# Kernel tuning notes

Hardware: AMD Instinct MI355X
Metric: run time of the kernel (lower is better)

## Reference

```python
import jax, jax.numpy as jnp
import numpy as np
from jax.scipy.special import logsumexp

B, T, V, E, H, L = 64, 256, 50000, 256, 256, 9


def setup_inputs() -> dict:
    key = jax.random.key(0)
    ks = jax.random.split(key, 10)
    lengths = jax.random.randint(ks[0], (B,), T // 2, T + 1)
    pm = jnp.arange(T)[None, :] < lengths[:, None]  # valid-token mask, padding at tail
    inp = jnp.where(pm, jax.random.randint(ks[1], (B, T), 1, V), 0).astype(jnp.int32)
    tags = jnp.where(pm, jax.random.randint(ks[2], (B, T), 0, L), 0).astype(jnp.int32)
    s = 0.05
    emb = jax.random.normal(ks[3], (V, E)) * s
    Wf = jax.random.normal(ks[4], (E, 4 * H)) * s
    Uf = jax.random.normal(ks[5], (H, 4 * H)) * s
    bf = jnp.zeros((4 * H,))
    Wb = jax.random.normal(ks[6], (E, 4 * H)) * s
    Ub = jax.random.normal(ks[7], (H, 4 * H)) * s
    bb = jnp.zeros((4 * H,))
    Wd = jax.random.normal(ks[8], (2 * H, L)) * s
    bd = jnp.zeros((L,))
    trans = jax.random.uniform(ks[9], (L, L))
    return dict(inp=inp, tags=tags, emb=emb, Wf=Wf, Uf=Uf, bf=bf,
                Wb=Wb, Ub=Ub, bb=bb, Wd=Wd, bd=bd, trans=trans)


def _lstm(x, mask, W, U, b):
    """Keras-style LSTM with masking (state + output carried through masked steps).
    x: [B,T,E], mask: [B,T] bool -> [B,T,H]."""
    h0 = jnp.zeros((x.shape[0], H), x.dtype)
    c0 = h0

    def step(carry, xm):
        h, c = carry
        xt, mt = xm
        z = xt @ W + h @ U + b  # [B,4H], gate order i,f,g,o (Keras)
        i, f, g, o = jnp.split(z, 4, axis=-1)
        c_new = jax.nn.sigmoid(f) * c + jax.nn.sigmoid(i) * jnp.tanh(g)
        h_new = jax.nn.sigmoid(o) * jnp.tanh(c_new)
        m = mt[:, None]
        h = jnp.where(m, h_new, h)
        c = jnp.where(m, c_new, c)
        return (h, c), h

    _, hs = jax.lax.scan(step, (h0, c0), (x.transpose(1, 0, 2), mask.T))
    return hs.transpose(1, 0, 2)


def _crf_log_likelihood(pot, tags, seq_lens, trans):
    """tfa.text.crf_log_likelihood: sequence_score - log_norm. pot: [B,T,L]."""
    Bv, Tv, Lv = pot.shape
    tmask = (jnp.arange(Tv)[None, :] < seq_lens[:, None]).astype(pot.dtype)
    unary = jnp.sum(jnp.take_along_axis(pot, tags[..., None], axis=-1)[..., 0] * tmask, axis=1)
    pmask = (jnp.arange(Tv - 1)[None, :] < (seq_lens - 1)[:, None]).astype(pot.dtype)
    binary = jnp.sum(trans[tags[:, :-1], tags[:, 1:]] * pmask, axis=1)

    # forward algorithm; alpha frozen once t >= seq_len (tfa uses dynamic_rnn semantics)
    def step(carry, pot_t):
        alpha, t = carry
        new = pot_t + logsumexp(alpha[:, :, None] + trans[None], axis=1)  # [B,L]
        alpha = jnp.where((t < seq_lens)[:, None], new, alpha)
        return (alpha, t + 1), None

    (alpha, _), _ = jax.lax.scan(step, (pot[:, 0, :], jnp.int32(1)),
                                 pot[:, 1:].transpose(1, 0, 2))
    log_norm = logsumexp(alpha, axis=-1)
    return unary + binary - log_norm


def reference(inp, tags, emb, Wf, Uf, bf, Wb, Ub, bb, Wd, bd, trans):
    mask = inp != 0
    seq_lens = jnp.sum(mask.astype(jnp.int32), axis=-1)
    x = jnp.take(emb, inp, axis=0)  # [B,T,E]; dropout is identity (inference)
    hf = _lstm(x, mask, Wf, Uf, bf)
    hb = _lstm(x[:, ::-1], mask[:, ::-1], Wb, Ub, bb)[:, ::-1]
    pot = jnp.concatenate([hf, hb], axis=-1) @ Wd + bd  # [B,T,L]
    ll = _crf_log_likelihood(pot, tags, seq_lens, trans)
    loss = -jnp.mean(ll / seq_lens.astype(pot.dtype))
    return pot, seq_lens, loss
```

## Files before the change

### kernel.cpp

```cpp
#include <hip/hip_runtime.h>

#define B_ 64
#define T_ 256
#define E_ 256
#define H_ 256
#define G4 1024
#define L_ 9

typedef __attribute__((ext_vector_type(8))) short bf16x8;
typedef __attribute__((ext_vector_type(4))) float f32x4;
typedef __attribute__((ext_vector_type(4))) unsigned uint4v;
typedef _Float16 half2v __attribute__((ext_vector_type(2)));

__device__ __forceinline__ ushort f2bf(float x){
  unsigned u = __float_as_uint(x);
  unsigned r = (u + 0x7FFFu + ((u >> 16) & 1u)) >> 16;
  return (ushort)r;
}
__device__ __forceinline__ float bf2f(unsigned u16v){
  return __uint_as_float(u16v << 16);
}
__device__ __forceinline__ float fsig(float x){
  return __builtin_amdgcn_rcpf(1.f + __expf(-x));
}
__device__ __forceinline__ float ftanh(float x){
  return 1.f - 2.f * __builtin_amdgcn_rcpf(__expf(2.f * x) + 1.f);
}
__device__ __forceinline__ int sdot4(unsigned a, unsigned b, int c){
#if __has_builtin(__builtin_amdgcn_sdot4)
  return __builtin_amdgcn_sdot4((int)a, (int)b, c, false);
#else
  int r = c;
  #pragma unroll
  for (int j = 0; j < 4; j++){
    int av = (int)(signed char)((a >> (8 * j)) & 0xFF);
    int bv = (int)(signed char)((b >> (8 * j)) & 0xFF);
    r += av * bv;
  }
  return r;
#endif
}

__global__ void k_prep(const int* __restrict__ inp, const float* __restrict__ emb,
                       const float* __restrict__ Wf, const float* __restrict__ Wb,
                       const float* __restrict__ Uf, const float* __restrict__ Ub,
                       ushort* __restrict__ WT, unsigned* __restrict__ Uq,
                       float* __restrict__ su, ushort* __restrict__ X,
                       int* __restrict__ lens, float* __restrict__ out_len){
  int bid = blockIdx.x, tid = threadIdx.x;
  if (bid < 2048){
    int idx = bid * 256 + tid;
    int dir = idx >> 18; int rem = idx & 262143;
    int np = rem >> 8, k = rem & 255;
    int c = ((np & 3) << 8) | (np >> 2);
    const float* W = dir ? Wb : Wf;
    WT[idx] = f2bf(W[k * G4 + c]);
  } else if (bid < 2080){
    int idx = bid - 2048;
    int dir = idx >> 4, blk = idx & 15;
    int c0 = blk * 64;
    int g = blk >> 2, u0 = (blk & 3) * 64;
    const float* U = dir ? Ub : Uf;
    int cp = tid & 63, ph = tid >> 6;
    __shared__ float redA[4][64];
    __shared__ float rs[64];
    __shared__ unsigned qbuf[64][64];
    float am = 0.f;
    for (int kk = 0; kk < 64; ++kk){
      float v = U[(size_t)(kk * 4 + ph) * G4 + c0 + cp];
      am = fmaxf(am, fabsf(v));
    }
    redA[ph][cp] = am;
    __syncthreads();
    if (tid < 64){
      float m = fmaxf(fmaxf(redA[0][tid], redA[1][tid]),
                      fmaxf(redA[2][tid], redA[3][tid]));
      float mm = fmaxf(m, 1e-20f);
      rs[tid] = 127.f / mm;
      su[dir * 1024 + c0 + tid] = mm * (1.f / 127.f);
    }
    __syncthreads();
    float rsv = rs[cp];
    for (int w = 0; w < 16; ++w){
      int kq = ph * 16 + w;
      unsigned word = 0;
      #pragma unroll
      for (int j = 0; j < 4; ++j){
        float v = U[(size_t)(kq * 4 + j) * G4 + c0 + cp];
        int q = __float2int_rn(v * rsv);
        q = max(-127, min(127, q));
        word |= ((unsigned)(q & 0xFF)) << (8 * j);
      }
      qbuf[kq][cp] = word;
    }
    __syncthreads();
    {
      int uu = tid >> 2, part = tid & 3;
      int kh = part >> 1, hs = part & 1;
      unsigned* dst = Uq + dir * 65536 + (u0 + uu) * 256 + kh * 128 + g * 32 + hs * 16;
      #pragma unroll
      for (int w4 = 0; w4 < 4; ++w4){
        int kb = kh * 32 + hs * 16 + w4 * 4;
        uint4 val;
        val.x = qbuf[kb + 0][uu];
        val.y = qbuf[kb + 1][uu];
        val.z = qbuf[kb + 2][uu];
        val.w = qbuf[kb + 3][uu];
        *(uint4*)(dst + w4 * 4) = val;
      }
    }
  } else if (bid < 4128){
    int idx = (bid - 2080) * 256 + tid;
    int m = idx >> 5, koff = (idx & 31) * 8;
    int tok = inp[m];
    const float* src = emb + (size_t)tok * E_ + koff;
    float4 a = *(const float4*)src;
    float4 b = *(const float4*)(src + 4);
    uint4 o;
    o.x = (unsigned)f2bf(a.x) | ((unsigned)f2bf(a.y) << 16);
    o.y = (unsigned)f2bf(a.z) | ((unsigned)f2bf(a.w) << 16);
    o.z = (unsigned)f2bf(b.x) | ((unsigned)f2bf(b.y) << 16);
    o.w = (unsigned)f2bf(b.z) | ((unsigned)f2bf(b.w) << 16);
    *(uint4*)(X + m * E_ + koff) = o;
  } else {
    int w = tid >> 6, lane = tid & 63;
    int b = (bid - 4128) * 4 + w;
    int c = 0;
    for (int t = lane; t < T_; t += 64) c += (inp[b * T_ + t] != 0);
    for (int off = 32; off; off >>= 1) c += __shfl_xor(c, off);
    if (lane == 0){ lens[b] = c; out_len[b] = (float)c; }
  }
}

__global__ __launch_bounds__(256) void k_gemm(const ushort* __restrict__ X,
        const ushort* __restrict__ WT, const float* __restrict__ bf_,
        const float* __restrict__ bb_, ushort* __restrict__ Zpf, ushort* __restrict__ Zpb){
  int zi = blockIdx.z;
  const ushort* wt = WT + zi * 262144;
  const float* bias = zi ? bb_ : bf_;
  ushort* Zp = zi ? Zpb : Zpf;
  int m0 = blockIdx.x * 128, n0 = blockIdx.y * 128;
  __shared__ ushort As[128 * 32];
  __shared__ ushort Bs[128 * 32];
  int tid = threadIdx.x;
  int lane = tid & 63, w = tid >> 6;
  int wr = w >> 1, wc = w & 1;
  int srow = lane >> 2, skq = lane & 3;
  int lr = lane & 15, kf8 = (lane >> 4) * 8;
  f32x4 acc[4][4] = {};
  for (int k0 = 0; k0 < E_; k0 += 32){
    #pragma unroll
    for (int j = 0; j < 2; j++){
      int rg = (w * 2 + j) * 16;
      const ushort* ga = X  + (size_t)(m0 + rg + srow) * E_ + k0 + skq * 8;
      const ushort* gb = wt + (size_t)(n0 + rg + srow) * E_ + k0 + skq * 8;
      __builtin_amdgcn_global_load_lds(
          (const __attribute__((address_space(1))) unsigned*)ga,
          (__attribute__((address_space(3))) unsigned*)&As[rg * 32], 16, 0, 0);
      __builtin_amdgcn_global_load_lds(
          (const __attribute__((address_space(1))) unsigned*)gb,
          (__attribute__((address_space(3))) unsigned*)&Bs[rg * 32], 16, 0, 0);
    }
    __syncthreads();
    bf16x8 af[4], bfr[4];
    #pragma unroll
    for (int i = 0; i < 4; i++){
      af[i]  = *(const bf16x8*)&As[(wr * 64 + i * 16 + lr) * 32 + kf8];
      bfr[i] = *(const bf16x8*)&Bs[(wc * 64 + i * 16 + lr) * 32 + kf8];
    }
    #pragma unroll
    for (int i = 0; i < 4; i++)
      #pragma unroll
      for (int j = 0; j < 4; j++)
        acc[i][j] = __builtin_amdgcn_mfma_f32_16x16x32_bf16(af[i], bfr[j], acc[i][j], 0, 0, 0);
    __syncthreads();
  }
  int crow = (lane >> 4) * 4;
  #pragma unroll
  for (int j = 0; j < 4; j++){
    int col = n0 + wc * 64 + j * 16 + lr;
    float bv = bias[((col & 3) << 8) | (col >> 2)];
    #pragma unroll
    for (int i = 0; i < 4; i++){
      int rbase = m0 + wr * 64 + i * 16 + crow;
      #pragma unroll
      for (int r = 0; r < 4; r++)
        Zp[(size_t)(rbase + r) * 1024 + col] = f2bf(acc[i][j][r] + bv);
    }
  }
}

__global__ __launch_bounds__(512, 2) void k_recur13(
    const ushort* __restrict__ Zpf, const ushort* __restrict__ Zpb,
    const unsigned* __restrict__ Uq, const float* __restrict__ su,
    const int* __restrict__ lens, ushort* __restrict__ hf16, ushort* __restrict__ hb16){
  int bid = blockIdx.x;
  int dir = bid >> 6, b = bid & 63;
  const uint2* Zp = (const uint2*)(dir ? Zpb : Zpf);
  ushort* H = dir ? hb16 : hf16;
  int tid = threadIdx.x;
  int u = tid >> 1, khalf = tid & 1;
  float sc0 = su[dir * 1024 +        u] * (1.f / 127.f);
  float sc1 = su[dir * 1024 + 256 +  u] * (1.f / 127.f);
  float sc2 = su[dir * 1024 + 512 +  u] * (1.f / 127.f);
  float sc3 = su[dir * 1024 + 768 +  u] * (1.f / 127.f);
  int alen = lens[b];

  uint4v uq[4][8];
  {
    const unsigned* p = Uq + dir * 65536 + u * 256 + khalf * 128;
    #pragma unroll
    for (int g = 0; g < 4; g++)
      #pragma unroll
      for (int i = 0; i < 8; i++)
        asm volatile("global_load_dwordx4 %0, %1, off"
                     : "=v"(uq[g][i]) : "v"(p + g * 32 + i * 4));
    asm volatile("s_waitcnt vmcnt(0)" ::: "memory");
    __builtin_amdgcn_sched_barrier(0);
  }

  __shared__ unsigned hq[2][64];
  if (tid < 128) ((unsigned*)hq)[tid] = 0u;
  __syncthreads();

  float c_st = 0.f, h_st = 0.f;
  int t0 = dir ? 255 : 0;
  uint2 zw = Zp[(size_t)(b * 256 + t0) * 256 + u];

  for (int s_ = 0; s_ < 256; ++s_){
    int t = dir ? (255 - s_) : s_;
    int tn = dir ? (t - 1) : (t + 1);
    int cur = s_ & 1, nxt = cur ^ 1;
    uint2 zw_n = uint2{0u, 0u};
    if (s_ < 255) zw_n = Zp[(size_t)(b * 256 + tn) * 256 + u];
    const uint4* hp = (const uint4*)&hq[cur][khalf * 32];
    uint4 hv[8];
    #pragma unroll
    for (int i = 0; i < 8; i++) hv[i] = hp[i];
    __builtin_amdgcn_sched_barrier(0);
    int a0 = 0, a1 = 0, a2 = 0, a3 = 0;
    #pragma unroll
    for (int i = 0; i < 8; i++){
      uint4 hvv = hv[i];
      a0 = sdot4(uq[0][i][0], hvv.x, a0);  a0 = sdot4(uq[0][i][1], hvv.y, a0);
      a0 = sdot4(uq[0][i][2], hvv.z, a0);  a0 = sdot4(uq[0][i][3], hvv.w, a0);
      a1 = sdot4(uq[1][i][0], hvv.x, a1);  a1 = sdot4(uq[1][i][1], hvv.y, a1);
      a1 = sdot4(uq[1][i][2], hvv.z, a1);  a1 = sdot4(uq[1][i][3], hvv.w, a1);
      a2 = sdot4(uq[2][i][0], hvv.x, a2);  a2 = sdot4(uq[2][i][1], hvv.y, a2);
      a2 = sdot4(uq[2][i][2], hvv.z, a2);  a2 = sdot4(uq[2][i][3], hvv.w, a2);
      a3 = sdot4(uq[3][i][0], hvv.x, a3);  a3 = sdot4(uq[3][i][1], hvv.y, a3);
      a3 = sdot4(uq[3][i][2], hvv.z, a3);  a3 = sdot4(uq[3][i][3], hvv.w, a3);
    }
    a0 += __shfl_xor(a0, 1);
    a1 += __shfl_xor(a1, 1);
    a2 += __shfl_xor(a2, 1);
    a3 += __shfl_xor(a3, 1);
    float zi = bf2f(zw.x & 0xffffu) + (float)a0 * sc0;
    float zf = bf2f(zw.x >> 16)     + (float)a1 * sc1;
    float zg = bf2f(zw.y & 0xffffu) + (float)a2 * sc2;
    float zo = bf2f(zw.y >> 16)     + (float)a3 * sc3;
    if (t < alen){
      c_st = fsig(zf) * c_st + fsig(zi) * ftanh(zg);
      h_st = fsig(zo) * ftanh(c_st);
    }
    if (khalf == 0){
      int ri = __float2int_rn(h_st * 127.f);
      ((char*)hq[nxt])[u] = (char)ri;
      H[(size_t)(b * 256 + t) * H_ + u] = f2bf(h_st);
    }
    __syncthreads();
    zw = zw_n;
  }
}

__global__ __launch_bounds__(256) void k_pot(const ushort* __restrict__ hf16,
        const ushort* __restrict__ hb16, const float* __restrict__ Wd,
        const float* __restrict__ bd, float* __restrict__ out, int* __restrict__ cnt){
  if (blockIdx.x == 0 && threadIdx.x == 0) *cnt = 0;
  int lane = threadIdx.x & 63, wid = threadIdx.x >> 6;
  int m = blockIdx.x * 4 + wid;
  uint2 ua = *(const uint2*)&hf16[(size_t)m * H_ + lane * 4];
  uint2 ub = *(const uint2*)&hb16[(size_t)m * H_ + lane * 4];
  float av[4] = {bf2f(ua.x & 0xFFFFu), bf2f(ua.x >> 16), bf2f(ua.y & 0xFFFFu), bf2f(ua.y >> 16)};
  float bv[4] = {bf2f(ub.x & 0xFFFFu), bf2f(ub.x >> 16), bf2f(ub.y & 0xFFFFu), bf2f(ub.y >> 16)};
  float acc[9];
  #pragma unroll
  for (int l = 0; l < 9; l++) acc[l] = 0.f;
  #pragma unroll
  for (int i = 0; i < 4; i++){
    int r = lane * 4 + i;
    #pragma unroll
    for (int l = 0; l < 9; l++)
      acc[l] += av[i] * Wd[r * 9 + l] + bv[i] * Wd[(H_ + r) * 9 + l];
  }
  #pragma unroll
  for (int off = 32; off; off >>= 1)
    #pragma unroll
    for (int l = 0; l < 9; l++) acc[l] += __shfl_xor(acc[l], off);
  if (lane == 0){
    #pragma unroll
    for (int l = 0; l < 9; l++) out[(size_t)m * 9 + l] = acc[l] + bd[l];
  }
}

__global__ void k_post(const float* __restrict__ out, const int* __restrict__ tags,
                       const float* __restrict__ trans, const int* __restrict__ lens,
                       float* __restrict__ lln, int* cnt, float* __restrict__ loss_out){
  int b = blockIdx.x, lane = threadIdx.x;
  int len = lens[b];
  const float* pot = out + (size_t)b * T_ * 9;
  float up = 0.f, bp = 0.f;
  for (int t = lane; t < T_; t += 64){
    int tg = tags[b * T_ + t];
    if (t < len) up += pot[t * 9 + tg];
    if (t + 1 < len){
      int tg2 = tags[b * T_ + t + 1];
      bp += trans[tg * 9 + tg2];
    }
  }
  for (int off = 32; off; off >>= 1){ up += __shfl_xor(up, off); bp += __shfl_xor(bp, off); }
  float alpha = 0.f;
  if (lane < 9){
    float tr[9];
    #pragma unroll
    for (int i = 0; i < 9; i++) tr[i] = trans[i * 9 + lane];
    alpha = pot[lane];
    for (int t = 1; t < T_; ++t){
      float v[9];
      #pragma unroll
      for (int i = 0; i < 9; i++) v[i] = __shfl(alpha, i) + tr[i];
      float mx = v[0];
      #pragma unroll
      for (int i = 1; i < 9; i++) mx = fmaxf(mx, v[i]);
      float sum = 0.f;
      #pragma unroll
      for (int i = 0; i < 9; i++) sum += __expf(v[i] - mx);
      float an = pot[t * 9 + lane] + mx + __logf(sum);
      if (t < len) alpha = an;
    }
  }
  float mx2 = -3.4e38f;
  for (int i = 0; i < 9; i++){ float a = __shfl(alpha, i); mx2 = fmaxf(mx2, a); }
  float s2 = 0.f;
  for (int i = 0; i < 9; i++){ float a = __shfl(alpha, i); s2 += __expf(a - mx2); }
  float lse = mx2 + __logf(s2);
  __shared__ int lastf;
  if (lane == 0){
    __hip_atomic_store(&lln[b], (up + bp - lse) / (float)len,
                       __ATOMIC_RELAXED, __HIP_MEMORY_SCOPE_AGENT);
    int old = __hip_atomic_fetch_add(cnt, 1, __ATOMIC_ACQ_REL, __HIP_MEMORY_SCOPE_AGENT);
    lastf = (old == 63);
  }
  __syncthreads();
  if (lastf){
    float v = __hip_atomic_load(&lln[lane], __ATOMIC_RELAXED, __HIP_MEMORY_SCOPE_AGENT);
    for (int off = 32; off; off >>= 1) v += __shfl_xor(v, off);
    if (lane == 0) loss_out[0] = -v * (1.f / 64.f);
  }
}

extern "C" void kernel_launch(void* const* d_in, const int* in_sizes, int n_in,
                              void* d_out, int out_size, void* d_ws, size_t ws_size,
                              hipStream_t stream) {
  (void)in_sizes; (void)n_in; (void)out_size; (void)ws_size;
  const int*   inp   = (const int*)  d_in[0];
  const int*   tags  = (const int*)  d_in[1];
  const float* emb   = (const float*)d_in[2];
  const float* Wf    = (const float*)d_in[3];
  const float* Uf    = (const float*)d_in[4];
  const float* bfv   = (const float*)d_in[5];
  const float* Wb    = (const float*)d_in[6];
  const float* Ub    = (const float*)d_in[7];
  const float* bbv   = (const float*)d_in[8];
  const float* Wd    = (const float*)d_in[9];
  const float* bd    = (const float*)d_in[10];
  const float* trans = (const float*)d_in[11];
  float* out = (float*)d_out;

  char* ws = (char*)d_ws;
  unsigned* Uq   = (unsigned*)(ws);
  float*    su   = (float*)   (ws + 524288);
  ushort*   WT16 = (ushort*)  (ws + 1048576);
  ushort*   Xbf  = (ushort*)  (ws + 2097152);
  int*      cnt  = (int*)     (ws + 2097152);
  ushort*   Zpf  = (ushort*)  (ws + 10485760);
  ushort*   Zpb  = (ushort*)  (ws + 44040192);
  ushort*   hf16 = (ushort*)  (ws + 77594624);
  ushort*   hb16 = (ushort*)  (ws + 85983232);
  int*      lens = (int*)     (ws + 94371840);
  float*    lln  = (float*)   (ws + 94372096);

  k_prep<<<4144, 256, 0, stream>>>(inp, emb, Wf, Wb, Uf, Ub, WT16, Uq, su, Xbf,
                                   lens, out + 147456);
  k_gemm<<<dim3(128, 8, 2), 256, 0, stream>>>(Xbf, WT16, bfv, bbv, Zpf, Zpb);
  k_recur13<<<128, 512, 0, stream>>>(Zpf, Zpb, Uq, su, lens, hf16, hb16);
  k_pot<<<4096, 256, 0, stream>>>(hf16, hb16, Wd, bd, out, cnt);
  k_post<<<64, 64, 0, stream>>>(out, tags, trans, lens, lln, cnt, out + 147520);
}
```

Baseline: 392.7 us.

## Fuse potential projection with CRF tail and stage GEMM output through LDS

Merges the emission-potential projection and the CRF forward/loss kernel into a single per-sequence kernel. Each block keeps its potentials in shared memory, so one launch and the global round-trip of potentials go away. The GEMM epilogue now writes the bf16 tile to padded LDS and then stores coalesced 16-byte rows instead of scattered 2-byte stores. The fused kernel runs only 64 blocks, so the projection gets far less parallelism than the 4096-block version had, and the GEMM block uses about 34KB more LDS. The counter reset moves into the prep kernel.

```diff
diff --git a/kernel.cpp b/kernel.cpp
--- a/kernel.cpp
+++ b/kernel.cpp
@@ -46,7 +46,8 @@
                        const float* __restrict__ Uf, const float* __restrict__ Ub,
                        ushort* __restrict__ WT, unsigned* __restrict__ Uq,
                        float* __restrict__ su, ushort* __restrict__ X,
-                       int* __restrict__ lens, float* __restrict__ out_len){
+                       int* __restrict__ lens, float* __restrict__ out_len,
+                       int* __restrict__ cnt){
   int bid = blockIdx.x, tid = threadIdx.x;
   if (bid < 2048){
     int idx = bid * 256 + tid;
@@ -123,6 +124,7 @@
     o.w = (unsigned)f2bf(b.z) | ((unsigned)f2bf(b.w) << 16);
     *(uint4*)(X + m * E_ + koff) = o;
   } else {
+    if (bid == 4128 && tid == 0) cnt[0] = 0;
     int w = tid >> 6, lane = tid & 63;
     int b = (bid - 4128) * 4 + w;
     int c = 0;
@@ -142,6 +144,7 @@
   int m0 = blockIdx.x * 128, n0 = blockIdx.y * 128;
   __shared__ ushort As[128 * 32];
   __shared__ ushort Bs[128 * 32];
+  __shared__ ushort Cs[128 * 136];
   int tid = threadIdx.x;
   int lane = tid & 63, w = tid >> 6;
   int wr = w >> 1, wc = w & 1;
@@ -178,15 +181,23 @@
   int crow = (lane >> 4) * 4;
   #pragma unroll
   for (int j = 0; j < 4; j++){
-    int col = n0 + wc * 64 + j * 16 + lr;
-    float bv = bias[((col & 3) << 8) | (col >> 2)];
+    int col = wc * 64 + j * 16 + lr;
+    float bv = bias[(((n0 + col) & 3) << 8) | ((n0 + col) >> 2)];
     #pragma unroll
     for (int i = 0; i < 4; i++){
-      int rbase = m0 + wr * 64 + i * 16 + crow;
+      int rbase = wr * 64 + i * 16 + crow;
       #pragma unroll
       for (int r = 0; r < 4; r++)
-        Zp[(size_t)(rbase + r) * 1024 + col] = f2bf(acc[i][j][r] + bv);
-    }
+        Cs[(rbase + r) * 136 + col] = f2bf(acc[i][j][r] + bv);
+    }
+  }
+  __syncthreads();
+  #pragma unroll
+  for (int P = 0; P < 8; P++){
+    int row = P * 16 + (tid >> 4);
+    int seg = tid & 15;
+    uint4 v = *(const uint4*)&Cs[row * 136 + seg * 8];
+    *(uint4*)&Zp[(size_t)(m0 + row) * 1024 + n0 + seg * 8] = v;
   }
 }
 
@@ -273,89 +284,96 @@
   }
 }
 
-__global__ __launch_bounds__(256) void k_pot(const ushort* __restrict__ hf16,
-        const ushort* __restrict__ hb16, const float* __restrict__ Wd,
-        const float* __restrict__ bd, float* __restrict__ out, int* __restrict__ cnt){
-  if (blockIdx.x == 0 && threadIdx.x == 0) *cnt = 0;
-  int lane = threadIdx.x & 63, wid = threadIdx.x >> 6;
-  int m = blockIdx.x * 4 + wid;
-  uint2 ua = *(const uint2*)&hf16[(size_t)m * H_ + lane * 4];
-  uint2 ub = *(const uint2*)&hb16[(size_t)m * H_ + lane * 4];
-  float av[4] = {bf2f(ua.x & 0xFFFFu), bf2f(ua.x >> 16), bf2f(ua.y & 0xFFFFu), bf2f(ua.y >> 16)};
-  float bv[4] = {bf2f(ub.x & 0xFFFFu), bf2f(ub.x >> 16), bf2f(ub.y & 0xFFFFu), bf2f(ub.y >> 16)};
-  float acc[9];
-  #pragma unroll
-  for (int l = 0; l < 9; l++) acc[l] = 0.f;
-  #pragma unroll
-  for (int i = 0; i < 4; i++){
-    int r = lane * 4 + i;
-    #pragma unroll
-    for (int l = 0; l < 9; l++)
-      acc[l] += av[i] * Wd[r * 9 + l] + bv[i] * Wd[(H_ + r) * 9 + l];
-  }
-  #pragma unroll
-  for (int off = 32; off; off >>= 1)
-    #pragma unroll
-    for (int l = 0; l < 9; l++) acc[l] += __shfl_xor(acc[l], off);
-  if (lane == 0){
-    #pragma unroll
-    for (int l = 0; l < 9; l++) out[(size_t)m * 9 + l] = acc[l] + bd[l];
-  }
-}
-
-__global__ void k_post(const float* __restrict__ out, const int* __restrict__ tags,
-                       const float* __restrict__ trans, const int* __restrict__ lens,
-                       float* __restrict__ lln, int* cnt, float* __restrict__ loss_out){
-  int b = blockIdx.x, lane = threadIdx.x;
-  int len = lens[b];
-  const float* pot = out + (size_t)b * T_ * 9;
-  float up = 0.f, bp = 0.f;
-  for (int t = lane; t < T_; t += 64){
-    int tg = tags[b * T_ + t];
-    if (t < len) up += pot[t * 9 + tg];
-    if (t + 1 < len){
-      int tg2 = tags[b * T_ + t + 1];
-      bp += trans[tg * 9 + tg2];
-    }
-  }
-  for (int off = 32; off; off >>= 1){ up += __shfl_xor(up, off); bp += __shfl_xor(bp, off); }
-  float alpha = 0.f;
-  if (lane < 9){
-    float tr[9];
-    #pragma unroll
-    for (int i = 0; i < 9; i++) tr[i] = trans[i * 9 + lane];
-    alpha = pot[lane];
-    for (int t = 1; t < T_; ++t){
-      float v[9];
-      #pragma unroll
-      for (int i = 0; i < 9; i++) v[i] = __shfl(alpha, i) + tr[i];
-      float mx = v[0];
-      #pragma unroll
-      for (int i = 1; i < 9; i++) mx = fmaxf(mx, v[i]);
-      float sum = 0.f;
-      #pragma unroll
-      for (int i = 0; i < 9; i++) sum += __expf(v[i] - mx);
-      float an = pot[t * 9 + lane] + mx + __logf(sum);
-      if (t < len) alpha = an;
-    }
-  }
-  float mx2 = -3.4e38f;
-  for (int i = 0; i < 9; i++){ float a = __shfl(alpha, i); mx2 = fmaxf(mx2, a); }
-  float s2 = 0.f;
-  for (int i = 0; i < 9; i++){ float a = __shfl(alpha, i); s2 += __expf(a - mx2); }
-  float lse = mx2 + __logf(s2);
-  __shared__ int lastf;
-  if (lane == 0){
-    __hip_atomic_store(&lln[b], (up + bp - lse) / (float)len,
-                       __ATOMIC_RELAXED, __HIP_MEMORY_SCOPE_AGENT);
-    int old = __hip_atomic_fetch_add(cnt, 1, __ATOMIC_ACQ_REL, __HIP_MEMORY_SCOPE_AGENT);
-    lastf = (old == 63);
+__global__ __launch_bounds__(1024) void k_tail(
+    const ushort* __restrict__ hf16, const ushort* __restrict__ hb16,
+    const float* __restrict__ Wd, const float* __restrict__ bd,
+    const int* __restrict__ tags, const float* __restrict__ trans,
+    const int* __restrict__ lens, float* __restrict__ out,
+    float* __restrict__ lln, int* cnt, float* __restrict__ loss_out){
+  int b = blockIdx.x;
+  int tid = threadIdx.x;
+  int lane = tid & 63, w = tid >> 6;
+  __shared__ float potS[256][9];
+  for (int it = 0; it < 16; ++it){
+    int r = w * 16 + it;
+    size_t m = (size_t)b * 256 + r;
+    uint2 ua = *(const uint2*)&hf16[m * 256 + lane * 4];
+    uint2 ub = *(const uint2*)&hb16[m * 256 + lane * 4];
+    float av[4] = {bf2f(ua.x & 0xFFFFu), bf2f(ua.x >> 16), bf2f(ua.y & 0xFFFFu), bf2f(ua.y >> 16)};
+    float bv[4] = {bf2f(ub.x & 0xFFFFu), bf2f(ub.x >> 16), bf2f(ub.y & 0xFFFFu), bf2f(ub.y >> 16)};
+    float acc[9];
+    #pragma unroll
+    for (int l = 0; l < 9; l++) acc[l] = 0.f;
+    #pragma unroll
+    for (int i = 0; i < 4; i++){
+      int rr = lane * 4 + i;
+      #pragma unroll
+      for (int l = 0; l < 9; l++)
+        acc[l] += av[i] * Wd[rr * 9 + l] + bv[i] * Wd[(H_ + rr) * 9 + l];
+    }
+    #pragma unroll
+    for (int off = 32; off; off >>= 1)
+      #pragma unroll
+      for (int l = 0; l < 9; l++) acc[l] += __shfl_xor(acc[l], off);
+    if (lane == 0){
+      #pragma unroll
+      for (int l = 0; l < 9; l++){
+        float v = acc[l] + bd[l];
+        potS[r][l] = v;
+        out[m * 9 + l] = v;
+      }
+    }
   }
   __syncthreads();
-  if (lastf){
-    float v = __hip_atomic_load(&lln[lane], __ATOMIC_RELAXED, __HIP_MEMORY_SCOPE_AGENT);
-    for (int off = 32; off; off >>= 1) v += __shfl_xor(v, off);
-    if (lane == 0) loss_out[0] = -v * (1.f / 64.f);
+  if (tid < 64){
+    int len = lens[b];
+    float up = 0.f, bp = 0.f;
+    for (int t = lane; t < T_; t += 64){
+      int tg = tags[b * T_ + t];
+      if (t < len) up += potS[t][tg];
+      if (t + 1 < len){
+        int tg2 = tags[b * T_ + t + 1];
+        bp += trans[tg * 9 + tg2];
+      }
+    }
+    for (int off = 32; off; off >>= 1){ up += __shfl_xor(up, off); bp += __shfl_xor(bp, off); }
+    float alpha = 0.f;
+    if (lane < 9){
+      float tr[9];
+      #pragma unroll
+      for (int i = 0; i < 9; i++) tr[i] = trans[i * 9 + lane];
+      alpha = potS[0][lane];
+      for (int t = 1; t < T_; ++t){
+        float v[9];
+        #pragma unroll
+        for (int i = 0; i < 9; i++) v[i] = __shfl(alpha, i) + tr[i];
+        float mx = v[0];
+        #pragma unroll
+        for (int i = 1; i < 9; i++) mx = fmaxf(mx, v[i]);
+        float sum = 0.f;
+        #pragma unroll
+        for (int i = 0; i < 9; i++) sum += __expf(v[i] - mx);
+        float an = potS[t][lane] + mx + __logf(sum);
+        if (t < len) alpha = an;
+      }
+    }
+    float mx2 = -3.4e38f;
+    for (int i = 0; i < 9; i++){ float a = __shfl(alpha, i); mx2 = fmaxf(mx2, a); }
+    float s2 = 0.f;
+    for (int i = 0; i < 9; i++){ float a = __shfl(alpha, i); s2 += __expf(a - mx2); }
+    float lse = mx2 + __logf(s2);
+    __shared__ int lastf;
+    if (lane == 0){
+      __hip_atomic_store(&lln[b], (up + bp - lse) / (float)len,
+                         __ATOMIC_RELAXED, __HIP_MEMORY_SCOPE_AGENT);
+      int old = __hip_atomic_fetch_add(cnt, 1, __ATOMIC_ACQ_REL, __HIP_MEMORY_SCOPE_AGENT);
+      lastf = (old == 63);
+    }
+    if (__shfl(lastf, 0)){
+      float v = __hip_atomic_load(&lln[lane], __ATOMIC_RELAXED, __HIP_MEMORY_SCOPE_AGENT);
+      for (int off = 32; off; off >>= 1) v += __shfl_xor(v, off);
+      if (lane == 0) loss_out[0] = -v * (1.f / 64.f);
+    }
   }
 }
 
@@ -382,18 +400,18 @@
   float*    su   = (float*)   (ws + 524288);
   ushort*   WT16 = (ushort*)  (ws + 1048576);
   ushort*   Xbf  = (ushort*)  (ws + 2097152);
-  int*      cnt  = (int*)     (ws + 2097152);
   ushort*   Zpf  = (ushort*)  (ws + 10485760);
   ushort*   Zpb  = (ushort*)  (ws + 44040192);
   ushort*   hf16 = (ushort*)  (ws + 77594624);
   ushort*   hb16 = (ushort*)  (ws + 85983232);
   int*      lens = (int*)     (ws + 94371840);
   float*    lln  = (float*)   (ws + 94372096);
+  int*      cnt  = (int*)     (ws + 94372352);
 
   k_prep<<<4144, 256, 0, stream>>>(inp, emb, Wf, Wb, Uf, Ub, WT16, Uq, su, Xbf,
-                                   lens, out + 147456);
+                                   lens, out + 147456, cnt);
   k_gemm<<<dim3(128, 8, 2), 256, 0, stream>>>(Xbf, WT16, bfv, bbv, Zpf, Zpb);
   k_recur13<<<128, 512, 0, stream>>>(Zpf, Zpb, Uq, su, lens, hf16, hb16);
-  k_pot<<<4096, 256, 0, stream>>>(hf16, hb16, Wd, bd, out, cnt);
-  k_post<<<64, 64, 0, stream>>>(out, tags, trans, lens, lln, cnt, out + 147520);
-}
+  k_tail<<<64, 1024, 0, stream>>>(hf16, hb16, Wd, bd, tags, trans, lens,
+                                  out, lln, cnt, out + 147520);
+}
```

After: 414.5 us. 5.6% more time.
